# Optimization experiments

Hardware: AMD Instinct MI355X
Metric: run time of the kernel (lower is better)

## Reference

```python
import jax, jax.numpy as jnp
import numpy as np

B, F, H, C = 256, 512, 1024, 1000
LN_EPS = 1e-5


def _proj(x, W, b, g, be):
    # AdaptiveAvgPool2d(1) + Flatten + Linear + LayerNorm + GELU(exact)
    p = x.mean(axis=(2, 3))                       # [B, Cin]
    h = p @ W + b                                 # [B, F]
    mu = h.mean(axis=-1, keepdims=True)
    var = h.var(axis=-1, keepdims=True)           # ddof=0, matches torch LayerNorm
    h = (h - mu) / jnp.sqrt(var + LN_EPS) * g + be
    return jax.nn.gelu(h, approximate=False)


def setup_inputs() -> dict:
    key = jax.random.key(0)
    ks = iter(jax.random.split(key, 64))
    def rn(shape, s=1.0):
        return jax.random.normal(next(ks), shape, jnp.float32) * s
    inp = {}
    feats = {"s1": (16, 112), "s2": (24, 56), "s3": (40, 28), "s4": (80, 14), "s5": (160, 7)}
    for n, (c, hw) in feats.items():
        inp[n] = rn((B, c, hw, hw))
    inp["ff"] = rn((B, 960, 7, 7))
    for i, c in enumerate([16, 24, 40, 80, 160], start=1):
        inp[f"Wp{i}"] = rn((c, F), 0.02)
        inp[f"bp{i}"] = jnp.zeros((F,), jnp.float32)
        inp[f"g{i}"] = jnp.ones((F,), jnp.float32)
        inp[f"be{i}"] = jnp.zeros((F,), jnp.float32)
    inp["Wg1"] = rn((960, H), 0.02); inp["bg1"] = jnp.zeros((H,), jnp.float32)
    inp["Wg2"] = rn((H, H // 2), 0.02); inp["bg2"] = jnp.zeros((H // 2,), jnp.float32)
    inp["Wg3"] = rn((H // 2, 5), 0.02); inp["bg3"] = jnp.zeros((5,), jnp.float32)
    inp["Wc1"] = rn((F, H), 0.02); inp["bc1"] = jnp.zeros((H,), jnp.float32)
    inp["Wc2"] = rn((H, H // 2), 0.02); inp["bc2"] = jnp.zeros((H // 2,), jnp.float32)
    inp["Wc3"] = rn((H // 2, C), 0.02); inp["bc3"] = jnp.zeros((C,), jnp.float32)
    return inp


def reference(s1, s2, s3, s4, s5, ff,
              Wp1, bp1, g1, be1, Wp2, bp2, g2, be2, Wp3, bp3, g3, be3,
              Wp4, bp4, g4, be4, Wp5, bp5, g5, be5,
              Wg1, bg1, Wg2, bg2, Wg3, bg3,
              Wc1, bc1, Wc2, bc2, Wc3, bc3):
    # gate on pooled final backbone features (dropout inactive at eval)
    gate_in = ff.mean(axis=(2, 3))                         # [B, 960]
    h = jax.nn.relu(gate_in @ Wg1 + bg1)
    h = jax.nn.relu(h @ Wg2 + bg2)
    gate_logits = h @ Wg3 + bg3                            # [B, 5]

    # per-stage projections -> [B, 5, F]
    stack = jnp.stack([
        _proj(s1, Wp1, bp1, g1, be1),
        _proj(s2, Wp2, bp2, g2, be2),
        _proj(s3, Wp3, bp3, g3, be3),
        _proj(s4, Wp4, bp4, g4, be4),
        _proj(s5, Wp5, bp5, g5, be5),
    ], axis=1)

    topv, topi = jax.lax.top_k(gate_logits, 2)             # [B, 2]
    w = jax.nn.softmax(topv, axis=1)                       # softmax over top-k logits
    sel = jnp.take_along_axis(stack, topi[:, :, None], axis=1)  # [B, 2, F]
    mixture = (sel * w[:, :, None]).sum(axis=1)            # [B, F]

    h = jax.nn.relu(mixture @ Wc1 + bc1)
    h = jax.nn.relu(h @ Wc2 + bc2)
    logits = h @ Wc3 + bc3                                 # [B, C]
    return logits, gate_logits, topi, w
```

## Files before the change

kernel.cpp:

```cpp
#include <hip/hip_runtime.h>
#include <math.h>


struct Pool4Segs {
    const float* src[4];
    float*       dst[4];
    int n4[4];
    int cum[4];
    float inv[4];
};

__global__ __launch_bounds__(256) void pool_big_kernel(Pool4Segs S, int total_waves) {
    int gid  = blockIdx.x * 256 + threadIdx.x;
    int wave = gid >> 6;
    int lane = gid & 63;
    if (wave >= total_waves) return;
    int s = 0;
    #pragma unroll
    for (int i = 0; i < 3; ++i) if (wave >= S.cum[i]) s = i + 1;
    int row = wave - (s == 0 ? 0 : S.cum[s - 1]);
    const int n4 = S.n4[s];
    const float4* p4 = (const float4*)(S.src[s]) + (size_t)row * n4;

    float a0 = 0.f, a1 = 0.f, a2 = 0.f, a3 = 0.f;
    float a4 = 0.f, a5 = 0.f, a6 = 0.f, a7 = 0.f;
    int k = lane;
    for (; k + 448 < n4; k += 512) {
        float4 v0 = p4[k];       float4 v1 = p4[k + 64];
        float4 v2 = p4[k + 128]; float4 v3 = p4[k + 192];
        float4 v4 = p4[k + 256]; float4 v5 = p4[k + 320];
        float4 v6 = p4[k + 384]; float4 v7 = p4[k + 448];
        a0 += (v0.x + v0.y) + (v0.z + v0.w);
        a1 += (v1.x + v1.y) + (v1.z + v1.w);
        a2 += (v2.x + v2.y) + (v2.z + v2.w);
        a3 += (v3.x + v3.y) + (v3.z + v3.w);
        a4 += (v4.x + v4.y) + (v4.z + v4.w);
        a5 += (v5.x + v5.y) + (v5.z + v5.w);
        a6 += (v6.x + v6.y) + (v6.z + v6.w);
        a7 += (v7.x + v7.y) + (v7.z + v7.w);
    }
    for (; k + 192 < n4; k += 256) {
        float4 v0 = p4[k];       float4 v1 = p4[k + 64];
        float4 v2 = p4[k + 128]; float4 v3 = p4[k + 192];
        a0 += (v0.x + v0.y) + (v0.z + v0.w);
        a1 += (v1.x + v1.y) + (v1.z + v1.w);
        a2 += (v2.x + v2.y) + (v2.z + v2.w);
        a3 += (v3.x + v3.y) + (v3.z + v3.w);
    }
    for (; k < n4; k += 64) {
        float4 v = p4[k];
        a0 += (v.x + v.y) + (v.z + v.w);
    }
    float acc = ((a0 + a1) + (a2 + a3)) + ((a4 + a5) + (a6 + a7));
    #pragma unroll
    for (int off = 32; off > 0; off >>= 1) acc += __shfl_down(acc, off, 64);
    if (lane == 0) S.dst[s][row] = acc * S.inv[s];
}

__global__ __launch_bounds__(256) void pool_small_kernel(const float* __restrict__ s5,
        const float* __restrict__ ff, float* __restrict__ dst5, float* __restrict__ dstf,
        int rows5) {
    __shared__ float lds[64 * 49];
    const int tid  = threadIdx.x;
    const int row0 = blockIdx.x * 64;
    const float* src;
    float* dst;
    int rbase;
    if (row0 < rows5) { src = s5; dst = dst5; rbase = row0; }
    else              { src = ff; dst = dstf; rbase = row0 - rows5; }
    const float4* p4 = (const float4*)(src + (size_t)rbase * 49);
    float4* l4 = (float4*)lds;
    float4 v0 = p4[tid];
    float4 v1 = p4[tid + 256];
    float4 v2 = p4[tid + 512];
    float4 v3;
    const bool t3 = (tid < 784 - 768);
    if (t3) v3 = p4[tid + 768];
    l4[tid]       = v0;
    l4[tid + 256] = v1;
    l4[tid + 512] = v2;
    if (t3) l4[tid + 768] = v3;
    __syncthreads();
    const int r  = tid >> 2;
    const int c0 = tid & 3;
    float s = 0.f;
    #pragma unroll
    for (int c = c0; c < 49; c += 4) s += lds[r * 49 + c];
    s += __shfl_down(s, 2, 64);
    s += __shfl_down(s, 1, 64);
    if (c0 == 0) dst[rbase + r] = s * (1.f / 49.f);
}

template <int ROWS>
__global__ __launch_bounds__(256) void fc_splitk_kernel(const float* __restrict__ X,
        const float* __restrict__ W, float* __restrict__ P,
        int M, int K, int N, int NW, int Kc, int total_waves) {
    int gid  = blockIdx.x * 256 + threadIdx.x;
    int wave = gid >> 6;
    int lane = gid & 63;
    if (wave >= total_waves) return;
    int wpk = (M / ROWS) * NW;
    int ks  = wave / wpk;
    int rem = wave - ks * wpk;
    int mg  = rem / NW;
    int nw  = rem - mg * NW;
    int n0  = nw * 256 + lane * 4;
    int m0  = mg * ROWS;
    const bool nok = (n0 < N);
    const int  n0s = nok ? n0 : 0;
    int k0 = ks * Kc;
    int k1 = k0 + Kc; if (k1 > K) k1 = K;
    const float* xp = X + (size_t)m0 * K;
    const float* wp = W + n0s;
    float4 acc[ROWS];
    #pragma unroll
    for (int r = 0; r < ROWS; ++r) acc[r] = make_float4(0.f, 0.f, 0.f, 0.f);
    #pragma unroll 4
    for (int k = k0; k < k1; ++k) {
        float4 w = *(const float4*)(wp + (size_t)k * N);
        #pragma unroll
        for (int r = 0; r < ROWS; ++r) {
            float x = xp[(size_t)r * K + k];
            acc[r].x += x * w.x; acc[r].y += x * w.y;
            acc[r].z += x * w.z; acc[r].w += x * w.w;
        }
    }
    if (!nok) return;
    float* pp = P + ((size_t)ks * M + m0) * N + n0;
    #pragma unroll
    for (int r = 0; r < ROWS; ++r) *(float4*)(pp + (size_t)r * N) = acc[r];
}

__global__ __launch_bounds__(256) void reduce_bias_kernel(const float* __restrict__ P,
        const float* __restrict__ bias, float* __restrict__ Y,
        int MN, int N, int KS, int do_relu) {
    int i = (blockIdx.x * 256 + threadIdx.x) * 4;
    if (i >= MN) return;
    float4 a = *(const float4*)(P + i);
    for (int s = 1; s < KS; ++s) {
        float4 b = *(const float4*)(P + (size_t)s * MN + i);
        a.x += b.x; a.y += b.y; a.z += b.z; a.w += b.w;
    }
    int n = i - (i / N) * N;
    float4 bb = *(const float4*)(bias + n);
    a.x += bb.x; a.y += bb.y; a.z += bb.z; a.w += bb.w;
    if (do_relu) {
        a.x = fmaxf(a.x, 0.f); a.y = fmaxf(a.y, 0.f);
        a.z = fmaxf(a.z, 0.f); a.w = fmaxf(a.w, 0.f);
    }
    *(float4*)(Y + i) = a;
}

__global__ __launch_bounds__(64) void fc3_top2_kernel(const float* __restrict__ X,
        const float* __restrict__ W, const float* __restrict__ bias,
        int* __restrict__ topi, float* __restrict__ wsm,
        float* __restrict__ out_gl, float* __restrict__ out_topi,
        float* __restrict__ out_w, int K) {
    const int b = blockIdx.x;
    const int lane = threadIdx.x;
    const float* x = X + (size_t)b * K;
    float acc[5] = {0.f, 0.f, 0.f, 0.f, 0.f};
    for (int k = lane; k < K; k += 64) {
        float xv = x[k];
        const float* wr = W + (size_t)k * 5;
        acc[0] += xv * wr[0]; acc[1] += xv * wr[1]; acc[2] += xv * wr[2];
        acc[3] += xv * wr[3]; acc[4] += xv * wr[4];
    }
    #pragma unroll
    for (int off = 32; off > 0; off >>= 1) {
        #pragma unroll
        for (int j = 0; j < 5; ++j) acc[j] += __shfl_down(acc[j], off, 64);
    }
    if (lane == 0) {
        float v[5];
        #pragma unroll
        for (int j = 0; j < 5; ++j) v[j] = acc[j] + bias[j];
        int i0 = 0;
        #pragma unroll
        for (int i = 1; i < 5; ++i) if (v[i] > v[i0]) i0 = i;
        int i1 = -1;
        #pragma unroll
        for (int i = 0; i < 5; ++i) {
            if (i == i0) continue;
            if (i1 < 0 || v[i] > v[i1]) i1 = i;
        }
        float e1 = __expf(v[i1] - v[i0]);
        float inv = 1.f / (1.f + e1);
        float w0 = inv, w1 = e1 * inv;
        topi[b * 2] = i0; topi[b * 2 + 1] = i1;
        wsm[b * 2] = w0;  wsm[b * 2 + 1] = w1;
        #pragma unroll
        for (int j = 0; j < 5; ++j) out_gl[b * 5 + j] = v[j];
        out_topi[b * 2]     = (float)i0;
        out_topi[b * 2 + 1] = (float)i1;
        out_w[b * 2]     = w0;
        out_w[b * 2 + 1] = w1;
    }
}

struct ProjParams {
    const float* W[5];
    const float* bp[5];
    const float* g[5];
    const float* be[5];
    int K[5];
    int poff[5];
};

__global__ __launch_bounds__(512) void proj_mix_kernel(ProjParams P,
        const float* __restrict__ pools, const int* __restrict__ topi,
        const float* __restrict__ wsm, float* __restrict__ mix) {
    const int b = blockIdx.x;
    const int f = threadIdx.x;
    __shared__ float sp[160];
    __shared__ float redS[8], redQ[8];
    __shared__ float s_mu, s_rstd;

    float acc = 0.f;
    for (int j = 0; j < 2; ++j) {
        __syncthreads();
        const int st = topi[b * 2 + j];
        const int K  = P.K[st];
        const float* p = pools + P.poff[st] + (size_t)b * K;
        if (f < K) sp[f] = p[f];
        __syncthreads();

        const float* W = P.W[st];
        float h = P.bp[st][f];
        #pragma unroll 4
        for (int k = 0; k < K; ++k) h += sp[k] * W[(size_t)k * 512 + f];

        float s = h, q = h * h;
        #pragma unroll
        for (int off = 32; off > 0; off >>= 1) {
            s += __shfl_down(s, off, 64);
            q += __shfl_down(q, off, 64);
        }
        const int lane = threadIdx.x & 63, wid = threadIdx.x >> 6;
        if (lane == 0) { redS[wid] = s; redQ[wid] = q; }
        __syncthreads();
        if (threadIdx.x == 0) {
            float ts = 0.f, tq = 0.f;
            #pragma unroll
            for (int i = 0; i < 8; ++i) { ts += redS[i]; tq += redQ[i]; }
            float mu  = ts * (1.f / 512.f);
            float var = tq * (1.f / 512.f) - mu * mu;
            s_mu   = mu;
            s_rstd = rsqrtf(var + 1e-5f);
        }
        __syncthreads();

        float x  = (h - s_mu) * s_rstd * P.g[st][f] + P.be[st][f];
        float ge = 0.5f * x * (1.f + erff(x * 0.70710678118654752f));
        acc += wsm[b * 2 + j] * ge;
    }
    mix[(size_t)b * 512 + f] = acc;
}

extern "C" void kernel_launch(void* const* d_in, const int* in_sizes, int n_in,
                              void* d_out, int out_size, void* d_ws, size_t ws_size,
                              hipStream_t stream) {
    const int B = 256, F = 512, H = 1024, C = 1000;

    const float* s1 = (const float*)d_in[0];
    const float* s2 = (const float*)d_in[1];
    const float* s3 = (const float*)d_in[2];
    const float* s4 = (const float*)d_in[3];
    const float* s5 = (const float*)d_in[4];
    const float* ff = (const float*)d_in[5];
    const float *Wp[5], *bp[5], *g[5], *be[5];
    for (int i = 0; i < 5; ++i) {
        Wp[i] = (const float*)d_in[6 + 4 * i];
        bp[i] = (const float*)d_in[7 + 4 * i];
        g[i]  = (const float*)d_in[8 + 4 * i];
        be[i] = (const float*)d_in[9 + 4 * i];
    }
    const float* Wg1 = (const float*)d_in[26]; const float* bg1 = (const float*)d_in[27];
    const float* Wg2 = (const float*)d_in[28]; const float* bg2 = (const float*)d_in[29];
    const float* Wg3 = (const float*)d_in[30]; const float* bg3 = (const float*)d_in[31];
    const float* Wc1 = (const float*)d_in[32]; const float* bc1 = (const float*)d_in[33];
    const float* Wc2 = (const float*)d_in[34]; const float* bc2 = (const float*)d_in[35];
    const float* Wc3 = (const float*)d_in[36]; const float* bc3 = (const float*)d_in[37];

    float* ws = (float*)d_ws;
    const int Ks[5]   = {16, 24, 40, 80, 160};
    const int poff[5] = {0, 4096, 10240, 20480, 40960};
    float* pools    = ws;
    float* gate_in  = ws + 81920;
    float* g1h      = ws + 327680;
    float* g2h      = ws + 589824;
    float* wsm      = ws + 722176;
    int*   topi     = (int*)(ws + 722688);
    float* mix      = ws + 723200;
    float* c1h      = ws + 854272;
    float* c2h      = ws + 1116416;
    float* partials = ws + 1247488;

    float* out      = (float*)d_out;
    float* out_gl   = out + 256000;
    float* out_topi = out + 257280;
    float* out_w    = out + 257792;

    Pool4Segs S;
    {
        const float* srcs[4] = { s1, s2, s3, s4 };
        float* dsts[4] = { pools + poff[0], pools + poff[1], pools + poff[2], pools + poff[3] };
        const int rls[4]  = { 112 * 112, 56 * 56, 28 * 28, 14 * 14 };
        const int rows[4] = { B * 16, B * 24, B * 40, B * 80 };
        int cum = 0;
        for (int i = 0; i < 4; ++i) {
            S.src[i] = srcs[i]; S.dst[i] = dsts[i]; S.n4[i] = rls[i] / 4;
            cum += rows[i]; S.cum[i] = cum; S.inv[i] = 1.f / rls[i];
        }
        int blocks = (cum * 64 + 255) / 256;
        pool_big_kernel<<<blocks, 256, 0, stream>>>(S, cum);
    }
    {
        int rows5 = B * 160;
        int total = rows5 + B * 960;
        pool_small_kernel<<<total / 64, 256, 0, stream>>>(s5, ff, pools + poff[4], gate_in, rows5);
    }

    auto fc = [&](const float* X, const float* W, const float* bias, float* Y,
                  int M, int K, int N, int KS, int do_relu) {
        int NW = (N + 255) / 256;
        int Kc = (K + KS - 1) / KS;
        int waves  = KS * (M / 2) * NW;
        int blocks = (waves * 64 + 255) / 256;
        fc_splitk_kernel<2><<<blocks, 256, 0, stream>>>(X, W, partials, M, K, N, NW, Kc, waves);
        int MN = M * N;
        reduce_bias_kernel<<<(MN / 4 + 255) / 256, 256, 0, stream>>>(
            partials, bias, Y, MN, N, KS, do_relu);
    };

    fc(gate_in, Wg1, bg1, g1h, B, 960, H, 4, 1);
    fc(g1h, Wg2, bg2, g2h, B, H, H / 2, 8, 1);
    fc3_top2_kernel<<<B, 64, 0, stream>>>(g2h, Wg3, bg3, topi, wsm,
                                          out_gl, out_topi, out_w, H / 2);

    ProjParams P;
    for (int i = 0; i < 5; ++i) {
        P.W[i] = Wp[i]; P.bp[i] = bp[i]; P.g[i] = g[i]; P.be[i] = be[i];
        P.K[i] = Ks[i]; P.poff[i] = poff[i];
    }
    proj_mix_kernel<<<B, 512, 0, stream>>>(P, pools, topi, wsm, mix);

    fc(mix, Wc1, bc1, c1h, B, F, H, 4, 1);
    fc(c1h, Wc2, bc2, c2h, B, H, H / 2, 8, 1);
    fc(c2h, Wc3, bc3, out, B, H / 2, C, 4, 0);
}
```

Baseline: 634.8 us.

## Vectorize split-K FC inner loop, raise rows per wave and split-K factor

```diff
diff --git a/kernel.cpp b/kernel.cpp
--- a/kernel.cpp
+++ b/kernel.cpp
@@ -115,14 +115,25 @@
     float4 acc[ROWS];
     #pragma unroll
     for (int r = 0; r < ROWS; ++r) acc[r] = make_float4(0.f, 0.f, 0.f, 0.f);
-    #pragma unroll 4
-    for (int k = k0; k < k1; ++k) {
-        float4 w = *(const float4*)(wp + (size_t)k * N);
+    #pragma unroll 2
+    for (int k = k0; k < k1; k += 4) {
+        float4 xv[ROWS];
+        #pragma unroll
+        for (int r = 0; r < ROWS; ++r)
+            xv[r] = *(const float4*)(xp + (size_t)r * K + k);
+        float4 w0 = *(const float4*)(wp + (size_t)(k + 0) * N);
+        float4 w1 = *(const float4*)(wp + (size_t)(k + 1) * N);
+        float4 w2 = *(const float4*)(wp + (size_t)(k + 2) * N);
+        float4 w3 = *(const float4*)(wp + (size_t)(k + 3) * N);
         #pragma unroll
         for (int r = 0; r < ROWS; ++r) {
-            float x = xp[(size_t)r * K + k];
-            acc[r].x += x * w.x; acc[r].y += x * w.y;
-            acc[r].z += x * w.z; acc[r].w += x * w.w;
+            float4 a = acc[r];
+            float4 x = xv[r];
+            a.x += x.x * w0.x; a.y += x.x * w0.y; a.z += x.x * w0.z; a.w += x.x * w0.w;
+            a.x += x.y * w1.x; a.y += x.y * w1.y; a.z += x.y * w1.z; a.w += x.y * w1.w;
+            a.x += x.z * w2.x; a.y += x.z * w2.y; a.z += x.z * w2.z; a.w += x.z * w2.w;
+            a.x += x.w * w3.x; a.y += x.w * w3.y; a.z += x.w * w3.z; a.w += x.w * w3.w;
+            acc[r] = a;
         }
     }
     if (!nok) return;
@@ -151,16 +162,19 @@
     *(float4*)(Y + i) = a;
 }
 
-__global__ __launch_bounds__(64) void fc3_top2_kernel(const float* __restrict__ X,
+__global__ __launch_bounds__(256) void fc3_top2_kernel(const float* __restrict__ X,
         const float* __restrict__ W, const float* __restrict__ bias,
         int* __restrict__ topi, float* __restrict__ wsm,
         float* __restrict__ out_gl, float* __restrict__ out_topi,
         float* __restrict__ out_w, int K) {
-    const int b = blockIdx.x;
-    const int lane = threadIdx.x;
+    const int b    = blockIdx.x;
+    const int tid  = threadIdx.x;
+    const int lane = tid & 63;
+    const int wv   = tid >> 6;
+    __shared__ float red[4][5];
     const float* x = X + (size_t)b * K;
     float acc[5] = {0.f, 0.f, 0.f, 0.f, 0.f};
-    for (int k = lane; k < K; k += 64) {
+    for (int k = tid; k < K; k += 256) {
         float xv = x[k];
         const float* wr = W + (size_t)k * 5;
         acc[0] += xv * wr[0]; acc[1] += xv * wr[1]; acc[2] += xv * wr[2];
@@ -172,9 +186,15 @@
         for (int j = 0; j < 5; ++j) acc[j] += __shfl_down(acc[j], off, 64);
     }
     if (lane == 0) {
+        #pragma unroll
+        for (int j = 0; j < 5; ++j) red[wv][j] = acc[j];
+    }
+    __syncthreads();
+    if (tid == 0) {
         float v[5];
         #pragma unroll
-        for (int j = 0; j < 5; ++j) v[j] = acc[j] + bias[j];
+        for (int j = 0; j < 5; ++j)
+            v[j] = ((red[0][j] + red[1][j]) + (red[2][j] + red[3][j])) + bias[j];
         int i0 = 0;
         #pragma unroll
         for (int i = 1; i < 5; ++i) if (v[i] > v[i0]) i0 = i;
@@ -226,9 +246,14 @@
         __syncthreads();
 
         const float* W = P.W[st];
-        float h = P.bp[st][f];
-        #pragma unroll 4
-        for (int k = 0; k < K; ++k) h += sp[k] * W[(size_t)k * 512 + f];
+        float h0 = 0.f, h1 = 0.f, h2 = 0.f, h3 = 0.f;
+        for (int k = 0; k < K; k += 4) {
+            h0 += sp[k]     * W[(size_t)(k)     * 512 + f];
+            h1 += sp[k + 1] * W[(size_t)(k + 1) * 512 + f];
+            h2 += sp[k + 2] * W[(size_t)(k + 2) * 512 + f];
+            h3 += sp[k + 3] * W[(size_t)(k + 3) * 512 + f];
+        }
+        float h = P.bp[st][f] + ((h0 + h1) + (h2 + h3));
 
         float s = h, q = h * h;
         #pragma unroll
@@ -294,7 +319,8 @@
     float* mix      = ws + 723200;
     float* c1h      = ws + 854272;
     float* c2h      = ws + 1116416;
-    float* partials = ws + 1247488;
+    const size_t part_off = 1247488;
+    float* partials = ws + part_off;
 
     float* out      = (float*)d_out;
     float* out_gl   = out + 256000;
@@ -322,21 +348,25 @@
     }
 
     auto fc = [&](const float* X, const float* W, const float* bias, float* Y,
-                  int M, int K, int N, int KS, int do_relu) {
+                  int M, int K, int N, int KSwant, int do_relu) {
         int NW = (N + 255) / 256;
-        int Kc = (K + KS - 1) / KS;
-        int waves  = KS * (M / 2) * NW;
+        size_t avail = ws_size / 4 > part_off ? ws_size / 4 - part_off : 0;
+        int KSmax = (int)(avail / ((size_t)M * N));
+        int KS = KSwant; if (KS > KSmax) KS = KSmax; if (KS < 1) KS = 1;
+        int Kc = (((K + KS - 1) / KS) + 3) & ~3;
+        KS = (K + Kc - 1) / Kc;
+        int waves  = KS * (M / 4) * NW;
         int blocks = (waves * 64 + 255) / 256;
-        fc_splitk_kernel<2><<<blocks, 256, 0, stream>>>(X, W, partials, M, K, N, NW, Kc, waves);
+        fc_splitk_kernel<4><<<blocks, 256, 0, stream>>>(X, W, partials, M, K, N, NW, Kc, waves);
         int MN = M * N;
         reduce_bias_kernel<<<(MN / 4 + 255) / 256, 256, 0, stream>>>(
             partials, bias, Y, MN, N, KS, do_relu);
     };
 
-    fc(gate_in, Wg1, bg1, g1h, B, 960, H, 4, 1);
-    fc(g1h, Wg2, bg2, g2h, B, H, H / 2, 8, 1);
-    fc3_top2_kernel<<<B, 64, 0, stream>>>(g2h, Wg3, bg3, topi, wsm,
-                                          out_gl, out_topi, out_w, H / 2);
+    fc(gate_in, Wg1, bg1, g1h, B, 960, H, 8, 1);
+    fc(g1h, Wg2, bg2, g2h, B, H, H / 2, 16, 1);
+    fc3_top2_kernel<<<B, 256, 0, stream>>>(g2h, Wg3, bg3, topi, wsm,
+                                           out_gl, out_topi, out_w, H / 2);
 
     ProjParams P;
     for (int i = 0; i < 5; ++i) {
@@ -345,7 +375,7 @@
     }
     proj_mix_kernel<<<B, 512, 0, stream>>>(P, pools, topi, wsm, mix);
 
-    fc(mix, Wc1, bc1, c1h, B, F, H, 4, 1);
-    fc(c1h, Wc2, bc2, c2h, B, H, H / 2, 8, 1);
-    fc(c2h, Wc3, bc3, out, B, H / 2, C, 4, 0);
-}
+    fc(mix, Wc1, bc1, c1h, B, F, H, 8, 1);
+    fc(c1h, Wc2, bc2, c2h, B, H, H / 2, 16, 1);
+    fc(c2h, Wc3, bc3, out, B, H / 2, C, 8, 0);
+}
```

Result: slower. 711.5 us (+12.1%).
